# Kernel optimization log

Hardware: AMD Instinct MI355X
Metric: run time of the kernel (lower is better)

## Reference

```python
import jax, jax.numpy as jnp
import numpy as np

N = 50000          # nodes
DEG = 16           # graph_max_neighbor
E = N * DEG        # edges (sorted by receiver)
DIM = 128          # config.hidden_dimension
EDGE_DIM = 32
EPS = 1e-5


def _ln(x, scale, offset, mask):
    # masked LayerNorm over last axis: normalize per row, then apply node mask
    m = jnp.mean(x, axis=-1, keepdims=True)
    v = jnp.mean(jnp.square(x - m), axis=-1, keepdims=True)
    return ((x - m) * jax.lax.rsqrt(v + EPS) * scale + offset) * mask


def setup_inputs() -> dict:
    key = jax.random.key(0)
    ks = jax.random.split(key, 12)
    node_inp = jax.random.normal(ks[0], (N, DIM), jnp.float32)
    edge_feat = jax.random.normal(ks[1], (E, EDGE_DIM), jnp.float32)
    node_mask = jnp.ones((N, 1), jnp.float32)
    senders = jax.random.randint(ks[2], (E,), 0, N, jnp.int32)
    receivers = jnp.repeat(jnp.arange(N, dtype=jnp.int32), DEG)  # sorted, DEG per node
    din_e = 2 * DIM + EDGE_DIM
    s = lambda d: 1.0 / np.sqrt(d)
    We1 = jax.random.normal(ks[3], (din_e, 2 * DIM), jnp.float32) * s(din_e)
    be1 = jnp.zeros((2 * DIM,), jnp.float32)
    We2 = jax.random.normal(ks[4], (2 * DIM, DIM), jnp.float32) * s(2 * DIM)
    be2 = jnp.zeros((DIM,), jnp.float32)
    g_msg = jnp.ones((DIM,), jnp.float32)
    b_msg = jnp.zeros((DIM,), jnp.float32)
    Wn1 = jax.random.normal(ks[5], (2 * DIM, 2 * DIM), jnp.float32) * s(2 * DIM)
    bn1 = jnp.zeros((2 * DIM,), jnp.float32)
    Wn2 = jax.random.normal(ks[6], (2 * DIM, DIM), jnp.float32) * s(2 * DIM)
    bn2 = jnp.zeros((DIM,), jnp.float32)
    g_node = jnp.ones((DIM,), jnp.float32)
    b_node = jnp.zeros((DIM,), jnp.float32)
    return dict(node_inp=node_inp, edge_feat=edge_feat, node_mask=node_mask,
                We1=We1, be1=be1, We2=We2, be2=be2, g_msg=g_msg, b_msg=b_msg,
                Wn1=Wn1, bn1=bn1, Wn2=Wn2, bn2=bn2, g_node=g_node, b_node=b_node,
                senders=senders, receivers=receivers)


def reference(node_inp, edge_feat, node_mask, We1, be1, We2, be2, g_msg, b_msg,
              Wn1, bn1, Wn2, bn2, g_node, b_node, senders, receivers):
    # gather + concat -> edge MLP (swish, no final activation; haiku MLP default)
    msg_input = jnp.concatenate(
        [node_inp[senders], node_inp[receivers], edge_feat], axis=-1)  # [E, 2*DIM+EDGE_DIM]
    h = jax.nn.swish(msg_input @ We1 + be1)
    messages = h @ We2 + be2                                           # [E, DIM]
    # scatter-reduce to receivers (sorted), mean over max neighbors
    agg = jax.ops.segment_sum(messages, receivers, num_segments=node_inp.shape[0],
                              indices_are_sorted=True) / DEG
    agg = _ln(agg, g_msg, b_msg, node_mask)
    # node update MLP + residual + masked LN
    nf = jnp.concatenate([node_inp, agg], axis=-1)                     # [N, 2*DIM]
    nf = jax.nn.swish(nf @ Wn1 + bn1) @ Wn2 + bn2                      # [N, DIM]
    nf = node_inp + nf
    return _ln(nf, g_node, b_node, node_mask)
```

## Files before the change

kernel.cpp:

```cpp
#include <hip/hip_runtime.h>

typedef _Float16 F16;
typedef _Float16 half8 __attribute__((ext_vector_type(8)));
typedef _Float16 half2 __attribute__((ext_vector_type(2)));
typedef float f32x4 __attribute__((ext_vector_type(4)));

#define N_NODES 50000
#define DEG 16
#define N_EDGES (N_NODES * DEG)
#define DIM 128

__device__ __forceinline__ float frcp(float x) { float r; asm("v_rcp_f32 %0, %1" : "=v"(r) : "v"(x)); return r; }
__device__ __forceinline__ float frsq(float x) { float r; asm("v_rsq_f32 %0, %1" : "=v"(r) : "v"(x)); return r; }
__device__ __forceinline__ float fexp2(float x) { float r; asm("v_exp_f32 %0, %1" : "=v"(r) : "v"(x)); return r; }
__device__ __forceinline__ float swishf(float x) { return x * frcp(1.0f + fexp2(x * -1.442695041f)); }

__device__ __forceinline__ half8 cvt8(f32x4 a, f32x4 b) {
    half8 h; h[0]=(F16)a[0]; h[1]=(F16)a[1]; h[2]=(F16)a[2]; h[3]=(F16)a[3];
    h[4]=(F16)b[0]; h[5]=(F16)b[1]; h[6]=(F16)b[2]; h[7]=(F16)b[3]; return h;
}

__device__ __forceinline__ void pack_one(const float* src, F16* dst, int idx,
                                         int K, int NC, int ld, int row0, int split) {
    int j = idx & 7;
    int l = (idx >> 3) & 63;
    int blob = idx >> 9;
    int ntiles = NC >> 4;
    int tcol = blob % ntiles;
    int c = blob / ntiles;
    int k = c * 32 + ((l >> 4) * 8) + j;
    int col = tcol * 16 + (l & 15);
    int sr = row0 + k, sc = col;
    if (split && col >= split) { sr += K; sc -= split; }
    dst[idx] = (F16)src[(size_t)sr * ld + sc];
}

__global__ void k_pack_all(const float* __restrict__ We1, const float* __restrict__ We2,
                           const float* __restrict__ Wn1, const float* __restrict__ Wn2,
                           F16* w1abp, F16* w1ep, F16* we2p, F16* wn1p, F16* wn2p) {
    int b = blockIdx.x, t = threadIdx.x;
    if (b < 256)      pack_one(We1, w1abp, (b - 0)   * 256 + t, 128, 512, 256, 0,   256);
    else if (b < 288) pack_one(We1, w1ep,  (b - 256) * 256 + t, 32,  256, 256, 256, 0);
    else if (b < 416) pack_one(We2, we2p,  (b - 288) * 256 + t, 256, 128, 128, 0,   0);
    else if (b < 672) pack_one(Wn1, wn1p,  (b - 416) * 256 + t, 256, 256, 256, 0,   0);
    else              pack_one(Wn2, wn2p,  (b - 672) * 256 + t, 256, 128, 128, 0,   0);
}

#define PAS 144
__global__ __launch_bounds__(256, 4) void k_proj(
    const float* __restrict__ node_inp, const float* __restrict__ be1,
    const F16* __restrict__ w1abp, F16* __restrict__ Ps, F16* __restrict__ Pr)
{
    __shared__ __align__(16) F16 A[64 * PAS];
    const int t = threadIdx.x;
    const int n0 = blockIdx.x * 64;

    #pragma unroll
    for (int i = 0; i < 4; ++i) {
        int id = t + i * 256; int row = id >> 4, c = id & 15;
        int gn = n0 + row; if (gn >= N_NODES) gn = N_NODES - 1;
        f32x4 v0 = *(const f32x4*)(node_inp + (size_t)gn * DIM + c * 8);
        f32x4 v1 = *(const f32x4*)(node_inp + (size_t)gn * DIM + c * 8 + 4);
        *(half8*)&A[row * PAS + c * 8] = cvt8(v0, v1);
    }
    __syncthreads();

    const int lane = t & 63, w = t >> 6;
    const int lcol = lane & 15, quad = lane >> 4;
    const int r0 = w * 16;

    #pragma unroll
    for (int half = 0; half < 2; ++half) {
        f32x4 acc[16] = {};
        #pragma unroll
        for (int c = 0; c < 4; ++c) {
            half8 a = *(const half8*)&A[(r0 + lcol) * PAS + c * 32 + quad * 8];
            const F16* wp = w1abp + (((size_t)(c * 32 + half * 16)) * 64 + lane) * 8;
            #pragma unroll
            for (int nt = 0; nt < 16; ++nt) {
                half8 bv = *(const half8*)(wp + (size_t)nt * 512);
                acc[nt] = __builtin_amdgcn_mfma_f32_16x16x32_f16(a, bv, acc[nt], 0, 0, 0);
            }
        }
        F16* dst = half ? Pr : Ps;
        #pragma unroll
        for (int nt = 0; nt < 16; ++nt) {
            int col = nt * 16 + lcol;
            float bias = half ? be1[col] : 0.0f;
            #pragma unroll
            for (int r = 0; r < 4; ++r) {
                int gn = n0 + r0 + quad * 4 + r;
                if (gn < N_NODES) dst[(size_t)gn * 256 + col] = (F16)(acc[nt][r] + bias);
            }
        }
    }
}

#define PGS 264
__global__ __launch_bounds__(64, 4) void k_edge(
    const F16* __restrict__ Ps, const F16* Pr,
    const float* __restrict__ edge_feat, const int* __restrict__ senders,
    const F16* __restrict__ w1ep, F16* Hm)
{
    __shared__ __align__(16) F16 Pg[16 * PGS];
    const int n = blockIdx.x;
    const int e0 = n * 16;
    const int lane = threadIdx.x;
    const int lcol = lane & 15, quad = lane >> 4;

    #pragma unroll
    for (int i = 0; i < 8; ++i) {
        int id = lane + i * 64; int row = id >> 5, c = id & 31;
        int s = senders[e0 + row];
        half8 ps = *(const half8*)(Ps + (size_t)s * 256 + c * 8);
        half8 pr = *(const half8*)(Pr + (size_t)n * 256 + c * 8);
        *(half8*)&Pg[row * PGS + c * 8] = ps + pr;
    }
    f32x4 v0 = *(const f32x4*)(edge_feat + (size_t)(e0 + lcol) * 32 + quad * 8);
    f32x4 v1 = *(const f32x4*)(edge_feat + (size_t)(e0 + lcol) * 32 + quad * 8 + 4);
    half8 a = cvt8(v0, v1);
    __syncthreads();

    #pragma unroll
    for (int h = 0; h < 2; ++h) {
        f32x4 acc[8] = {};
        #pragma unroll
        for (int j = 0; j < 8; ++j) {
            half8 bv = *(const half8*)(w1ep + (((size_t)(h * 8 + j)) * 64 + lane) * 8);
            acc[j] = __builtin_amdgcn_mfma_f32_16x16x32_f16(a, bv, acc[j], 0, 0, 0);
        }
        #pragma unroll
        for (int j = 0; j < 8; ++j) {
            int nt = h * 8 + j;
            const F16* pgp = &Pg[(quad * 4) * PGS + nt * 16 + lcol];
            float s = 0.f;
            #pragma unroll
            for (int r = 0; r < 4; ++r) {
                float x = acc[j][r] + (float)pgp[r * PGS];
                s += swishf(x);
            }
            s += __shfl_xor(s, 16, 64);
            s += __shfl_xor(s, 32, 64);
            if (lane < 16) Hm[(size_t)n * 256 + nt * 16 + lane] = (F16)(s * 0.0625f);
        }
    }
}

#define XS 272
#define FSS 137
__global__ __launch_bounds__(256, 4) void k_node(
    const float* __restrict__ node_inp, const F16* Hm,
    const float* __restrict__ be2, const float* __restrict__ g_msg, const float* __restrict__ b_msg,
    const float* __restrict__ bn1, const float* __restrict__ bn2,
    const float* __restrict__ g_node, const float* __restrict__ b_node,
    const float* __restrict__ node_mask,
    const F16* __restrict__ we2p, const F16* __restrict__ wn1p, const F16* __restrict__ wn2p,
    float* out)
{
    __shared__ __align__(16) unsigned char smem[64 * 274 * 2];
    F16* X = (F16*)smem;
    float* Fs = (float*)smem;

    const int t = threadIdx.x;
    const int n0 = blockIdx.x * 64;
    const int lane = t & 63, w = t >> 6;
    const int lcol = lane & 15, quad = lane >> 4;
    const int r0 = w * 16;

    #pragma unroll
    for (int i = 0; i < 4; ++i) {
        int id = lane + i * 64; int row = id >> 4, c = id & 15;
        int gn = n0 + r0 + row; if (gn >= N_NODES) gn = N_NODES - 1;
        f32x4 v0 = *(const f32x4*)(node_inp + (size_t)gn * DIM + c * 8);
        f32x4 v1 = *(const f32x4*)(node_inp + (size_t)gn * DIM + c * 8 + 4);
        *(half8*)&X[(r0 + row) * XS + c * 8] = cvt8(v0, v1);
    }

    {
        int gr = n0 + r0 + lcol; if (gr >= N_NODES) gr = N_NODES - 1;
        const F16* hrow = Hm + (size_t)gr * 256;
        f32x4 acc[8] = {};
        #pragma unroll
        for (int c = 0; c < 8; ++c) {
            half8 a = *(const half8*)(hrow + c * 32 + quad * 8);
            const F16* wp = we2p + (((size_t)(c * 8)) * 64 + lane) * 8;
            #pragma unroll
            for (int nt = 0; nt < 8; ++nt) {
                half8 bv = *(const half8*)(wp + (size_t)nt * 512);
                acc[nt] = __builtin_amdgcn_mfma_f32_16x16x32_f16(a, bv, acc[nt], 0, 0, 0);
            }
        }
        #pragma unroll
        for (int nt = 0; nt < 8; ++nt) {
            int col = nt * 16 + lcol;
            float b = be2[col];
            #pragma unroll
            for (int r = 0; r < 4; ++r)
                X[(r0 + quad * 4 + r) * XS + 128 + col] = (F16)(acc[nt][r] + b);
        }
    }
    __syncthreads();

    {
        int row = lane >> 2, q = lane & 3;
        int gn = n0 + r0 + row; if (gn >= N_NODES) gn = N_NODES - 1;
        float vv[32]; float sum = 0.f, sq = 0.f;
        #pragma unroll
        for (int j = 0; j < 4; ++j) {
            half8 hv = *(const half8*)&X[(r0 + row) * XS + 128 + q * 32 + j * 8];
            #pragma unroll
            for (int k = 0; k < 8; ++k) { float f = (float)hv[k]; vv[j*8+k] = f; sum += f; sq += f*f; }
        }
        sum += __shfl_xor(sum, 1, 64); sq += __shfl_xor(sq, 1, 64);
        sum += __shfl_xor(sum, 2, 64); sq += __shfl_xor(sq, 2, 64);
        float mean = sum * (1.0f / DIM);
        float rs = frsq(sq * (1.0f / DIM) - mean * mean + 1e-5f);
        float msk = node_mask[gn];
        #pragma unroll
        for (int j = 0; j < 16; ++j) {
            int col = q * 32 + j * 2;
            half2 o;
            o[0] = (F16)(((vv[j*2]   - mean) * rs * g_msg[col]   + b_msg[col])   * msk);
            o[1] = (F16)(((vv[j*2+1] - mean) * rs * g_msg[col+1] + b_msg[col+1]) * msk);
            *(half2*)&X[(r0 + row) * XS + 128 + col] = o;
        }
    }
    __syncthreads();

    {
        f32x4 acc1[16] = {};
        #pragma unroll
        for (int c = 0; c < 8; ++c) {
            half8 a = *(const half8*)&X[(r0 + lcol) * XS + c * 32 + quad * 8];
            const F16* wp = wn1p + (((size_t)(c * 16)) * 64 + lane) * 8;
            #pragma unroll
            for (int nt = 0; nt < 16; ++nt) {
                half8 bv = *(const half8*)(wp + (size_t)nt * 512);
                acc1[nt] = __builtin_amdgcn_mfma_f32_16x16x32_f16(a, bv, acc1[nt], 0, 0, 0);
            }
        }
        __syncthreads();
        #pragma unroll
        for (int nt = 0; nt < 16; ++nt) {
            int col = nt * 16 + lcol;
            float b = bn1[col];
            #pragma unroll
            for (int r = 0; r < 4; ++r) {
                float x = acc1[nt][r] + b;
                X[(r0 + quad * 4 + r) * XS + col] = (F16)swishf(x);
            }
        }
    }
    __syncthreads();

    {
        f32x4 acc2[8] = {};
        #pragma unroll
        for (int c = 0; c < 8; ++c) {
            half8 a = *(const half8*)&X[(r0 + lcol) * XS + c * 32 + quad * 8];
            const F16* wp = wn2p + (((size_t)(c * 8)) * 64 + lane) * 8;
            #pragma unroll
            for (int nt = 0; nt < 8; ++nt) {
                half8 bv = *(const half8*)(wp + (size_t)nt * 512);
                acc2[nt] = __builtin_amdgcn_mfma_f32_16x16x32_f16(a, bv, acc2[nt], 0, 0, 0);
            }
        }
        __syncthreads();
        #pragma unroll
        for (int nt = 0; nt < 8; ++nt) {
            int col = nt * 16 + lcol;
            float b = bn2[col];
            #pragma unroll
            for (int r = 0; r < 4; ++r)
                Fs[(r0 + quad * 4 + r) * FSS + col] = acc2[nt][r] + b;
        }
    }
    __syncthreads();

    {
        int row = lane >> 2, q = lane & 3;
        int gn = n0 + r0 + row;
        f32x4 xr[8];
        float sum = 0.f, sq = 0.f;
        if (gn < N_NODES) {
            #pragma unroll
            for (int j = 0; j < 8; ++j) {
                f32x4 aa = *(const f32x4*)&Fs[(r0 + row) * FSS + q * 32 + j * 4];
                f32x4 ni = *(const f32x4*)(node_inp + (size_t)gn * DIM + q * 32 + j * 4);
                f32x4 x = aa + ni;
                xr[j] = x;
                sum += x[0] + x[1] + x[2] + x[3];
                sq  += x[0]*x[0] + x[1]*x[1] + x[2]*x[2] + x[3]*x[3];
            }
        }
        sum += __shfl_xor(sum, 1, 64); sq += __shfl_xor(sq, 1, 64);
        sum += __shfl_xor(sum, 2, 64); sq += __shfl_xor(sq, 2, 64);
        if (gn < N_NODES) {
            float mean = sum * (1.0f / DIM);
            float rs = frsq(sq * (1.0f / DIM) - mean * mean + 1e-5f);
            float msk = node_mask[gn];
            #pragma unroll
            for (int j = 0; j < 8; ++j) {
                f32x4 o;
                #pragma unroll
                for (int qq = 0; qq < 4; ++qq) {
                    int col = q * 32 + j * 4 + qq;
                    o[qq] = ((xr[j][qq] - mean) * rs * g_node[col] + b_node[col]) * msk;
                }
                *(f32x4*)(out + (size_t)gn * DIM + q * 32 + j * 4) = o;
            }
        }
    }
}


extern "C" void kernel_launch(void* const* d_in, const int* in_sizes, int n_in,
                              void* d_out, int out_size, void* d_ws, size_t ws_size,
                              hipStream_t stream)
{
    const float* node_inp  = (const float*)d_in[0];
    const float* edge_feat = (const float*)d_in[1];
    const float* node_mask = (const float*)d_in[2];
    const float* We1 = (const float*)d_in[3];
    const float* be1 = (const float*)d_in[4];
    const float* We2 = (const float*)d_in[5];
    const float* be2 = (const float*)d_in[6];
    const float* g_msg = (const float*)d_in[7];
    const float* b_msg = (const float*)d_in[8];
    const float* Wn1 = (const float*)d_in[9];
    const float* bn1 = (const float*)d_in[10];
    const float* Wn2 = (const float*)d_in[11];
    const float* bn2 = (const float*)d_in[12];
    const float* g_node = (const float*)d_in[13];
    const float* b_node = (const float*)d_in[14];
    const int* senders = (const int*)d_in[15];
    float* out = (float*)d_out;

    char* ws = (char*)d_ws;
    F16* Ps = (F16*)ws;
    size_t off = (size_t)N_NODES * 256 * 2;
    F16* w1abp = (F16*)(ws + off); off += 128 * 512 * 2;
    F16* w1ep  = (F16*)(ws + off); off += 32 * 256 * 2;
    F16* we2p  = (F16*)(ws + off); off += 256 * 128 * 2;
    F16* wn1p  = (F16*)(ws + off); off += 256 * 256 * 2;
    F16* wn2p  = (F16*)(ws + off); off += 256 * 128 * 2;

    F16* PrHm = (F16*)d_out;

    k_pack_all<<<dim3(800), dim3(256), 0, stream>>>(We1, We2, Wn1, Wn2,
                                                    w1abp, w1ep, we2p, wn1p, wn2p);

    k_proj<<<dim3((N_NODES + 63) / 64), dim3(256), 0, stream>>>(node_inp, be1, w1abp, Ps, PrHm);

    k_edge<<<dim3(N_NODES), dim3(64), 0, stream>>>(Ps, PrHm, edge_feat, senders, w1ep, PrHm);

    k_node<<<dim3((N_NODES + 63) / 64), dim3(256), 0, stream>>>(
        node_inp, PrHm, be2, g_msg, b_msg, bn1, bn2, g_node, b_node, node_mask,
        we2p, wn1p, wn2p, out);
}
```

Baseline: 364.2 us.

## Re-tile projection and node GEMMs by column per wave, batch four nodes per edge block

k_proj and k_node now give each wave a slice of output columns across all 64 rows, instead of a slice of 16 rows across all columns. Each weight fragment loaded from global memory is therefore reused across four row tiles, which cuts redundant weight traffic. k_edge now handles four nodes per 256-thread block, stages sender indices in shared memory, and gathers each 128-column half just before it is used, which shrinks LDS use and block count. Shared-memory padding strides were also changed to reduce bank conflicts; k_proj drops to 2 blocks per CU, with more accumulator registers per wave.

Measured after the change: 362.8 us. About the same (-0.4%).

```diff
diff --git a/kernel.cpp b/kernel.cpp
--- a/kernel.cpp
+++ b/kernel.cpp
@@ -46,8 +46,8 @@
     else              pack_one(Wn2, wn2p,  (b - 672) * 256 + t, 256, 128, 128, 0,   0);
 }
 
-#define PAS 144
-__global__ __launch_bounds__(256, 4) void k_proj(
+#define PAS 152
+__global__ __launch_bounds__(256, 2) void k_proj(
     const float* __restrict__ node_inp, const float* __restrict__ be1,
     const F16* __restrict__ w1abp, F16* __restrict__ Ps, F16* __restrict__ Pr)
 {
@@ -65,64 +65,76 @@
     }
     __syncthreads();
 
-    const int lane = t & 63, w = t >> 6;
+    const int lane = t & 63, wn = t >> 6;
     const int lcol = lane & 15, quad = lane >> 4;
-    const int r0 = w * 16;
-
-    #pragma unroll
-    for (int half = 0; half < 2; ++half) {
-        f32x4 acc[16] = {};
-        #pragma unroll
-        for (int c = 0; c < 4; ++c) {
-            half8 a = *(const half8*)&A[(r0 + lcol) * PAS + c * 32 + quad * 8];
-            const F16* wp = w1abp + (((size_t)(c * 32 + half * 16)) * 64 + lane) * 8;
-            #pragma unroll
-            for (int nt = 0; nt < 16; ++nt) {
-                half8 bv = *(const half8*)(wp + (size_t)nt * 512);
-                acc[nt] = __builtin_amdgcn_mfma_f32_16x16x32_f16(a, bv, acc[nt], 0, 0, 0);
-            }
-        }
-        F16* dst = half ? Pr : Ps;
-        #pragma unroll
-        for (int nt = 0; nt < 16; ++nt) {
-            int col = nt * 16 + lcol;
-            float bias = half ? be1[col] : 0.0f;
+
+    f32x4 acc[4][8] = {};
+    #pragma unroll
+    for (int c = 0; c < 4; ++c) {
+        half8 af[4];
+        #pragma unroll
+        for (int rt = 0; rt < 4; ++rt)
+            af[rt] = *(const half8*)&A[(rt * 16 + lcol) * PAS + c * 32 + quad * 8];
+        const F16* wp = w1abp + (((size_t)(c * 32 + wn * 8)) * 64 + lane) * 8;
+        #pragma unroll
+        for (int nt = 0; nt < 8; ++nt) {
+            half8 bv = *(const half8*)(wp + (size_t)nt * 512);
+            #pragma unroll
+            for (int rt = 0; rt < 4; ++rt)
+                acc[rt][nt] = __builtin_amdgcn_mfma_f32_16x16x32_f16(af[rt], bv, acc[rt][nt], 0, 0, 0);
+        }
+    }
+
+    F16* dst = (wn < 2) ? Ps : Pr;
+    const int cb = (wn & 1) * 128;
+    #pragma unroll
+    for (int nt = 0; nt < 8; ++nt) {
+        int col = cb + nt * 16 + lcol;
+        float bias = (wn >= 2) ? be1[col] : 0.0f;
+        #pragma unroll
+        for (int rt = 0; rt < 4; ++rt) {
             #pragma unroll
             for (int r = 0; r < 4; ++r) {
-                int gn = n0 + r0 + quad * 4 + r;
-                if (gn < N_NODES) dst[(size_t)gn * 256 + col] = (F16)(acc[nt][r] + bias);
-            }
-        }
-    }
-}
-
-#define PGS 264
-__global__ __launch_bounds__(64, 4) void k_edge(
+                int gn = n0 + rt * 16 + quad * 4 + r;
+                if (gn < N_NODES) dst[(size_t)gn * 256 + col] = (F16)(acc[rt][nt][r] + bias);
+            }
+        }
+    }
+}
+
+#define PGS2 136
+__global__ __launch_bounds__(256, 4) void k_edge(
     const F16* __restrict__ Ps, const F16* Pr,
     const float* __restrict__ edge_feat, const int* __restrict__ senders,
     const F16* __restrict__ w1ep, F16* Hm)
 {
-    __shared__ __align__(16) F16 Pg[16 * PGS];
-    const int n = blockIdx.x;
-    const int e0 = n * 16;
-    const int lane = threadIdx.x;
+    __shared__ __align__(16) F16 Pg[4 * 16 * PGS2];
+    __shared__ int sidx[64];
+    const int t = threadIdx.x;
+    const int n0 = blockIdx.x * 4;
+    const int e0 = n0 * 16;
+    const int lane = t & 63, nd = t >> 6;
     const int lcol = lane & 15, quad = lane >> 4;
-
-    #pragma unroll
-    for (int i = 0; i < 8; ++i) {
-        int id = lane + i * 64; int row = id >> 5, c = id & 31;
-        int s = senders[e0 + row];
-        half8 ps = *(const half8*)(Ps + (size_t)s * 256 + c * 8);
-        half8 pr = *(const half8*)(Pr + (size_t)n * 256 + c * 8);
-        *(half8*)&Pg[row * PGS + c * 8] = ps + pr;
-    }
-    f32x4 v0 = *(const f32x4*)(edge_feat + (size_t)(e0 + lcol) * 32 + quad * 8);
-    f32x4 v1 = *(const f32x4*)(edge_feat + (size_t)(e0 + lcol) * 32 + quad * 8 + 4);
+    const int n = n0 + nd;
+
+    if (t < 64) sidx[t] = senders[e0 + t];
+
+    f32x4 v0 = *(const f32x4*)(edge_feat + (size_t)(e0 + nd * 16 + lcol) * 32 + quad * 8);
+    f32x4 v1 = *(const f32x4*)(edge_feat + (size_t)(e0 + nd * 16 + lcol) * 32 + quad * 8 + 4);
     half8 a = cvt8(v0, v1);
     __syncthreads();
 
+    F16* pg = &Pg[nd * 16 * PGS2];
     #pragma unroll
     for (int h = 0; h < 2; ++h) {
+        #pragma unroll
+        for (int i = 0; i < 4; ++i) {
+            int id = lane + i * 64; int row = id >> 4, c = id & 15;
+            int s = sidx[nd * 16 + row];
+            half8 ps = *(const half8*)(Ps + (size_t)s * 256 + h * 128 + c * 8);
+            half8 pr = *(const half8*)(Pr + (size_t)n * 256 + h * 128 + c * 8);
+            *(half8*)&pg[row * PGS2 + c * 8] = ps + pr;
+        }
         f32x4 acc[8] = {};
         #pragma unroll
         for (int j = 0; j < 8; ++j) {
@@ -131,23 +143,22 @@
         }
         #pragma unroll
         for (int j = 0; j < 8; ++j) {
-            int nt = h * 8 + j;
-            const F16* pgp = &Pg[(quad * 4) * PGS + nt * 16 + lcol];
+            const F16* pgp = &pg[(quad * 4) * PGS2 + j * 16 + lcol];
             float s = 0.f;
             #pragma unroll
             for (int r = 0; r < 4; ++r) {
-                float x = acc[j][r] + (float)pgp[r * PGS];
+                float x = acc[j][r] + (float)pgp[r * PGS2];
                 s += swishf(x);
             }
             s += __shfl_xor(s, 16, 64);
             s += __shfl_xor(s, 32, 64);
-            if (lane < 16) Hm[(size_t)n * 256 + nt * 16 + lane] = (F16)(s * 0.0625f);
-        }
-    }
-}
-
-#define XS 272
-#define FSS 137
+            if (lane < 16) Hm[(size_t)n * 256 + h * 128 + j * 16 + lane] = (F16)(s * 0.0625f);
+        }
+    }
+}
+
+#define XS 280
+#define FSS 139
 __global__ __launch_bounds__(256, 4) void k_node(
     const float* __restrict__ node_inp, const F16* Hm,
     const float* __restrict__ be2, const float* __restrict__ g_msg, const float* __restrict__ b_msg,
@@ -157,7 +168,7 @@
     const F16* __restrict__ we2p, const F16* __restrict__ wn1p, const F16* __restrict__ wn2p,
     float* out)
 {
-    __shared__ __align__(16) unsigned char smem[64 * 274 * 2];
+    __shared__ __align__(16) unsigned char smem[64 * XS * 2];
     F16* X = (F16*)smem;
     float* Fs = (float*)smem;
 
@@ -165,29 +176,29 @@
     const int n0 = blockIdx.x * 64;
     const int lane = t & 63, w = t >> 6;
     const int lcol = lane & 15, quad = lane >> 4;
-    const int r0 = w * 16;
 
     #pragma unroll
     for (int i = 0; i < 4; ++i) {
-        int id = lane + i * 64; int row = id >> 4, c = id & 15;
-        int gn = n0 + r0 + row; if (gn >= N_NODES) gn = N_NODES - 1;
+        int id = t + i * 256; int row = id >> 4, c = id & 15;
+        int gn = n0 + row; if (gn >= N_NODES) gn = N_NODES - 1;
         f32x4 v0 = *(const f32x4*)(node_inp + (size_t)gn * DIM + c * 8);
         f32x4 v1 = *(const f32x4*)(node_inp + (size_t)gn * DIM + c * 8 + 4);
-        *(half8*)&X[(r0 + row) * XS + c * 8] = cvt8(v0, v1);
-    }
-
-    {
+        *(half8*)&X[row * XS + c * 8] = cvt8(v0, v1);
+    }
+
+    {
+        const int r0 = w * 16;
         int gr = n0 + r0 + lcol; if (gr >= N_NODES) gr = N_NODES - 1;
         const F16* hrow = Hm + (size_t)gr * 256;
         f32x4 acc[8] = {};
         #pragma unroll
         for (int c = 0; c < 8; ++c) {
-            half8 a = *(const half8*)(hrow + c * 32 + quad * 8);
+            half8 af = *(const half8*)(hrow + c * 32 + quad * 8);
             const F16* wp = we2p + (((size_t)(c * 8)) * 64 + lane) * 8;
             #pragma unroll
             for (int nt = 0; nt < 8; ++nt) {
                 half8 bv = *(const half8*)(wp + (size_t)nt * 512);
-                acc[nt] = __builtin_amdgcn_mfma_f32_16x16x32_f16(a, bv, acc[nt], 0, 0, 0);
+                acc[nt] = __builtin_amdgcn_mfma_f32_16x16x32_f16(af, bv, acc[nt], 0, 0, 0);
             }
         }
         #pragma unroll
@@ -202,12 +213,12 @@
     __syncthreads();
 
     {
-        int row = lane >> 2, q = lane & 3;
-        int gn = n0 + r0 + row; if (gn >= N_NODES) gn = N_NODES - 1;
+        int row = t >> 2, q = t & 3;
+        int gn = n0 + row; if (gn >= N_NODES) gn = N_NODES - 1;
         float vv[32]; float sum = 0.f, sq = 0.f;
         #pragma unroll
         for (int j = 0; j < 4; ++j) {
-            half8 hv = *(const half8*)&X[(r0 + row) * XS + 128 + q * 32 + j * 8];
+            half8 hv = *(const half8*)&X[row * XS + 128 + q * 32 + j * 8];
             #pragma unroll
             for (int k = 0; k < 8; ++k) { float f = (float)hv[k]; vv[j*8+k] = f; sum += f; sq += f*f; }
         }
@@ -222,70 +233,84 @@
             half2 o;
             o[0] = (F16)(((vv[j*2]   - mean) * rs * g_msg[col]   + b_msg[col])   * msk);
             o[1] = (F16)(((vv[j*2+1] - mean) * rs * g_msg[col+1] + b_msg[col+1]) * msk);
-            *(half2*)&X[(r0 + row) * XS + 128 + col] = o;
-        }
-    }
-    __syncthreads();
-
-    {
-        f32x4 acc1[16] = {};
+            *(half2*)&X[row * XS + 128 + col] = o;
+        }
+    }
+    __syncthreads();
+
+    {
+        f32x4 acc1[4][4] = {};
         #pragma unroll
         for (int c = 0; c < 8; ++c) {
-            half8 a = *(const half8*)&X[(r0 + lcol) * XS + c * 32 + quad * 8];
-            const F16* wp = wn1p + (((size_t)(c * 16)) * 64 + lane) * 8;
-            #pragma unroll
-            for (int nt = 0; nt < 16; ++nt) {
+            half8 af[4];
+            #pragma unroll
+            for (int rt = 0; rt < 4; ++rt)
+                af[rt] = *(const half8*)&X[(rt * 16 + lcol) * XS + c * 32 + quad * 8];
+            const F16* wp = wn1p + (((size_t)(c * 16 + w * 4)) * 64 + lane) * 8;
+            #pragma unroll
+            for (int nt = 0; nt < 4; ++nt) {
                 half8 bv = *(const half8*)(wp + (size_t)nt * 512);
-                acc1[nt] = __builtin_amdgcn_mfma_f32_16x16x32_f16(a, bv, acc1[nt], 0, 0, 0);
+                #pragma unroll
+                for (int rt = 0; rt < 4; ++rt)
+                    acc1[rt][nt] = __builtin_amdgcn_mfma_f32_16x16x32_f16(af[rt], bv, acc1[rt][nt], 0, 0, 0);
             }
         }
         __syncthreads();
         #pragma unroll
-        for (int nt = 0; nt < 16; ++nt) {
-            int col = nt * 16 + lcol;
+        for (int nt = 0; nt < 4; ++nt) {
+            int col = w * 64 + nt * 16 + lcol;
             float b = bn1[col];
             #pragma unroll
-            for (int r = 0; r < 4; ++r) {
-                float x = acc1[nt][r] + b;
-                X[(r0 + quad * 4 + r) * XS + col] = (F16)swishf(x);
-            }
-        }
-    }
-    __syncthreads();
-
-    {
-        f32x4 acc2[8] = {};
+            for (int rt = 0; rt < 4; ++rt)
+                #pragma unroll
+                for (int r = 0; r < 4; ++r) {
+                    float x = acc1[rt][nt][r] + b;
+                    X[(rt * 16 + quad * 4 + r) * XS + col] = (F16)swishf(x);
+                }
+        }
+    }
+    __syncthreads();
+
+    {
+        f32x4 acc2[4][2] = {};
         #pragma unroll
         for (int c = 0; c < 8; ++c) {
-            half8 a = *(const half8*)&X[(r0 + lcol) * XS + c * 32 + quad * 8];
-            const F16* wp = wn2p + (((size_t)(c * 8)) * 64 + lane) * 8;
-            #pragma unroll
-            for (int nt = 0; nt < 8; ++nt) {
+            half8 af[4];
+            #pragma unroll
+            for (int rt = 0; rt < 4; ++rt)
+                af[rt] = *(const half8*)&X[(rt * 16 + lcol) * XS + c * 32 + quad * 8];
+            const F16* wp = wn2p + (((size_t)(c * 8 + w * 2)) * 64 + lane) * 8;
+            #pragma unroll
+            for (int nt = 0; nt < 2; ++nt) {
                 half8 bv = *(const half8*)(wp + (size_t)nt * 512);
-                acc2[nt] = __builtin_amdgcn_mfma_f32_16x16x32_f16(a, bv, acc2[nt], 0, 0, 0);
+                #pragma unroll
+                for (int rt = 0; rt < 4; ++rt)
+                    acc2[rt][nt] = __builtin_amdgcn_mfma_f32_16x16x32_f16(af[rt], bv, acc2[rt][nt], 0, 0, 0);
             }
         }
         __syncthreads();
         #pragma unroll
-        for (int nt = 0; nt < 8; ++nt) {
-            int col = nt * 16 + lcol;
+        for (int nt = 0; nt < 2; ++nt) {
+            int col = w * 32 + nt * 16 + lcol;
             float b = bn2[col];
             #pragma unroll
-            for (int r = 0; r < 4; ++r)
-                Fs[(r0 + quad * 4 + r) * FSS + col] = acc2[nt][r] + b;
-        }
-    }
-    __syncthreads();
-
-    {
-        int row = lane >> 2, q = lane & 3;
-        int gn = n0 + r0 + row;
+            for (int rt = 0; rt < 4; ++rt)
+                #pragma unroll
+                for (int r = 0; r < 4; ++r)
+                    Fs[(rt * 16 + quad * 4 + r) * FSS + col] = acc2[rt][nt][r] + b;
+        }
+    }
+    __syncthreads();
+
+    {
+        int row = t >> 2, q = t & 3;
+        int gn = n0 + row;
         f32x4 xr[8];
         float sum = 0.f, sq = 0.f;
         if (gn < N_NODES) {
             #pragma unroll
             for (int j = 0; j < 8; ++j) {
-                f32x4 aa = *(const f32x4*)&Fs[(r0 + row) * FSS + q * 32 + j * 4];
+                f32x4 aa = *(const f32x4*)&Fs[row * FSS + q * 32 + j * 4];
                 f32x4 ni = *(const f32x4*)(node_inp + (size_t)gn * DIM + q * 32 + j * 4);
                 f32x4 x = aa + ni;
                 xr[j] = x;
@@ -352,7 +377,7 @@
 
     k_proj<<<dim3((N_NODES + 63) / 64), dim3(256), 0, stream>>>(node_inp, be1, w1abp, Ps, PrHm);
 
-    k_edge<<<dim3(N_NODES), dim3(64), 0, stream>>>(Ps, PrHm, edge_feat, senders, w1ep, PrHm);
+    k_edge<<<dim3(N_NODES / 4), dim3(256), 0, stream>>>(Ps, PrHm, edge_feat, senders, w1ep, PrHm);
 
     k_node<<<dim3((N_NODES + 63) / 64), dim3(256), 0, stream>>>(
         node_inp, PrHm, be2, g_msg, b_msg, bn1, bn2, g_node, b_node, node_mask,
```
